# Kernel optimization log

Measured on AMD Instinct MI355X. Metric: run time of the kernel, lower is better.

The kernel has to match this reference:

```python
import jax, jax.numpy as jnp
import numpy as np

# Production-scale 3D conv: B=4, C=64->64, 32^3 volume, 3x3x3 kernel, stride 1, pad 1.
B, CIN, COUT = 4, 64, 64
KSIZE = (3, 3, 3)
STRIDE = (1, 1, 1)
PAD = 1
SPATIAL = (32, 32, 32)


def setup_inputs() -> dict:
    key = jax.random.key(0)
    k1, k2, k3 = jax.random.split(key, 3)
    x = jax.random.normal(k1, (B, CIN) + SPATIAL, dtype=jnp.float32)
    weight = jax.random.normal(k2, (COUT, CIN) + KSIZE, dtype=jnp.float32)
    bias = jax.random.normal(k3, (COUT,), dtype=jnp.float32)
    return {"x": x, "weight": weight, "bias": bias}


def reference(x, weight, bias):
    # The original materializes all sliding-window patches via nested unfold and
    # contracts with einsum('bci...,oci->bo...'). That is exactly a standard
    # cross-correlation (torch-style conv). We express the same math as a direct
    # convolution, avoiding the O(kernel_volume) patch blowup.
    out = jax.lax.conv_general_dilated(
        x,
        weight,
        window_strides=STRIDE,
        padding=[(PAD, PAD)] * 3,
        dimension_numbers=("NCDHW", "OIDHW", "NCDHW"),
    )
    return out + bias.reshape(1, -1, 1, 1, 1)
```

## Files before the change

kernel.cpp:

```cpp
#include <hip/hip_runtime.h>
#include <hip/hip_bf16.h>

#define WS_W_OFF    0
#define WS_ZERO_OFF 221184
#define WS_XT_OFF   262144

typedef __attribute__((ext_vector_type(8)))  short s16x8;
typedef __attribute__((ext_vector_type(4)))  float f32x4;
typedef __attribute__((ext_vector_type(16))) float f32x16;

#define GLOBAL_AS __attribute__((address_space(1)))
#define LDS_AS    __attribute__((address_space(3)))

__device__ __forceinline__ unsigned short f2bf(float f) {
  unsigned u = __builtin_bit_cast(unsigned, f);
  u = u + 0x7fffu + ((u >> 16) & 1u);
  return (unsigned short)(u >> 16);
}

__global__ void prep_kernel(const float* __restrict__ x,
                            const float* __restrict__ w,
                            unsigned short* __restrict__ wsw,
                            float* __restrict__ zeros,
                            unsigned short* __restrict__ xt) {
  int blk = blockIdx.x;
  if (blk < 432) {
    int t = blk * 256 + threadIdx.x;
    int tap  = t % 27;
    int cin  = (t / 27) & 63;
    int cout = t / (27 * 64);
    int h  = cin >> 5;
    int c5 = cin & 31;
    int ks = c5 >> 4;
    int hi = (c5 >> 3) & 1;
    int j  = c5 & 7;
    int nt = cout >> 5;
    int l  = hi * 32 + (cout & 31);
    int f  = nt * 2 + ks;
    int dst = (((tap * 2 + h) * 4 + f) * 64 + l) * 8 + j;
    wsw[dst] = f2bf(w[t]);
    if (t < 64) zeros[t] = 0.0f;
  } else {
    int t  = (blk - 432) * 256 + threadIdx.x;
    int s  = t & 32767;
    int c8 = (t >> 15) & 7;
    int b  = t >> 18;
    const float* src = x + (size_t)(b * 64 + c8 * 8) * 32768 + s;
    s16x8 v;
    #pragma unroll
    for (int k = 0; k < 8; ++k) v[k] = (short)f2bf(src[(size_t)k * 32768]);
    *(s16x8*)(xt + (size_t)(b * 32768 + s) * 64 + c8 * 8) = v;
  }
}

__global__ __launch_bounds__(256, 2) void conv_kernel(const float* __restrict__ bias,
                                                      float* __restrict__ out,
                                                      const char* __restrict__ ws) {
  __shared__ __align__(16) unsigned char halo[52 * 1024];

  const int tid  = threadIdx.x;
  const int lane = tid & 63;
  const int w    = tid >> 6;
  const int logical = (blockIdx.x & 7) * 64 + (blockIdx.x >> 3);
  const int yt = logical & 7, zt = (logical >> 3) & 15, b = logical >> 7;
  const int z0 = zt * 2, y0 = yt * 4;
  const int zo  = w >> 1;
  const int yo2 = (w & 1) * 2;

  const int q31 = lane & 31;
  const int hi  = lane >> 5;

  const int sl_sub   = lane >> 2;
  const int sl_chunk = (lane & 3) ^ ((lane >> 3) & 3);

  auto stage_halo = [&](int h) {
    for (int g = w; g < 52; g += 4) {
      int pos = g * 16 + sl_sub;
      int hz = pos / 204; int rem = pos - hz * 204;
      int hy = rem / 34;  int hx = rem - hy * 34;
      int gz = z0 + hz - 1, gy = y0 + hy - 1, gx = hx - 1;
      bool inb = (pos < 816) & ((unsigned)gz < 32u) &
                 ((unsigned)gy < 32u) & ((unsigned)gx < 32u);
      int s = (gz * 32 + gy) * 32 + gx;
      int src = inb ? (WS_XT_OFF + (b * 32768 + s) * 128 + h * 64 + sl_chunk * 16)
                    : WS_ZERO_OFF;
      __builtin_amdgcn_global_load_lds(
          (const GLOBAL_AS void*)(ws + src),
          (LDS_AS void*)(&halo[g * 1024 + lane * 16]),
          16, 0, 0);
    }
  };

  const s16x8* __restrict__ wfr = (const s16x8*)(ws + WS_W_OFF);

  f32x16 acc[2][2];
  #pragma unroll
  for (int mt = 0; mt < 2; ++mt)
    #pragma unroll
    for (int nt = 0; nt < 2; ++nt)
      #pragma unroll
      for (int r = 0; r < 16; ++r) acc[mt][nt][r] = 0.0f;

  s16x8 Ab[3][4], Bb[3][4];
  const int pA0 = (zo * 6 + yo2) * 34 + q31;
  const int pA1 = pA0 + 34;

  auto loadB = [&](int slot, int h, int tap) {
    #pragma unroll
    for (int f = 0; f < 4; ++f)
      Bb[slot][f] = wfr[((tap * 2 + h) * 4 + f) * 64 + lane];
  };

  auto loadA = [&](int slot, int tap) {
    const int kd = tap / 9, r9 = tap - kd * 9;
    const int kh = r9 / 3, kw = r9 - kh * 3;
    const int d  = (kd * 6 + kh) * 34 + kw;
    #pragma unroll
    for (int mt = 0; mt < 2; ++mt) {
      int p = (mt ? pA1 : pA0) + d;
      #pragma unroll
      for (int ks = 0; ks < 2; ++ks) {
        int swz = ((ks << 1) | hi) ^ ((p >> 1) & 3);
        Ab[slot][mt * 2 + ks] = *(const s16x8*)&halo[(p << 6) + (swz << 4)];
      }
    }
  };

  auto compute = [&](int slot) {
    #pragma unroll
    for (int ks = 0; ks < 2; ++ks)
      #pragma unroll
      for (int mt = 0; mt < 2; ++mt)
        #pragma unroll
        for (int nt = 0; nt < 2; ++nt)
          acc[mt][nt] = __builtin_amdgcn_mfma_f32_32x32x16_bf16(
              Ab[slot][mt * 2 + ks], Bb[slot][nt * 2 + ks], acc[mt][nt], 0, 0, 0);
  };

  auto run27 = [&](int h) {
    loadA(0, 0); loadA(1, 1);
    #pragma unroll
    for (int tap = 0; tap < 27; ++tap) {
      if (tap < 25) {
        loadB((tap + 2) % 3, h, tap + 2);
        loadA((tap + 2) % 3, tap + 2);
      }
      compute(tap % 3);
    }
  };

  stage_halo(0);
  loadB(0, 0, 0); loadB(1, 0, 1);
  __syncthreads();
  run27(0);

  loadB(0, 1, 0); loadB(1, 1, 1);
  __syncthreads();
  stage_halo(1);
  __syncthreads();
  run27(1);

  const int z = z0 + zo;
  #pragma unroll
  for (int nt = 0; nt < 2; ++nt) {
    int cout = nt * 32 + q31;
    float bv = bias[cout];
    #pragma unroll
    for (int mt = 0; mt < 2; ++mt) {
      int y = y0 + yo2 + mt;
      float* orow = out + ((size_t)((b * 64 + cout) * 32 + z) * 32 + y) * 32;
      #pragma unroll
      for (int q = 0; q < 4; ++q) {
        int x0 = q * 8 + hi * 4;
        f32x4 v;
        #pragma unroll
        for (int r = 0; r < 4; ++r) v[r] = acc[mt][nt][q * 4 + r] + bv;
        *(f32x4*)&orow[x0] = v;
      }
    }
  }
}

extern "C" void kernel_launch(void* const* d_in, const int* in_sizes, int n_in,
                              void* d_out, int out_size, void* d_ws, size_t ws_size,
                              hipStream_t stream) {
  const float* x    = (const float*)d_in[0];
  const float* wgt  = (const float*)d_in[1];
  const float* bias = (const float*)d_in[2];
  float* out = (float*)d_out;
  char* ws = (char*)d_ws;

  prep_kernel<<<4528, 256, 0, stream>>>(x, wgt,
                                        (unsigned short*)(ws + WS_W_OFF),
                                        (float*)(ws + WS_ZERO_OFF),
                                        (unsigned short*)(ws + WS_XT_OFF));
  conv_kernel<<<512, 256, 0, stream>>>(bias, out, ws);
}
```

Before: 50.05 us.

## Enlarge conv block tile to 4 z-planes with 8 waves splitting cout halves

Each block now covers 4 z × 4 y rows with 512 threads and 256 blocks. Each wave handles one z row, four y rows and one 32-wide cout half. The larger tile cuts the halo overlap, so less input is re-staged per output. The explicit triple-buffered register prefetch is removed in favour of per-tap loads, with s_setprio raised around the MFMA bursts. In exchange the kernel needs more LDS per block (about 78KB), and with only 256 blocks the grid may under-fill the GPU.

```diff
diff --git a/kernel.cpp b/kernel.cpp
--- a/kernel.cpp
+++ b/kernel.cpp
@@ -53,130 +53,105 @@
   }
 }
 
-__global__ __launch_bounds__(256, 2) void conv_kernel(const float* __restrict__ bias,
+__global__ __launch_bounds__(512, 2) void conv_kernel(const float* __restrict__ bias,
                                                       float* __restrict__ out,
                                                       const char* __restrict__ ws) {
-  __shared__ __align__(16) unsigned char halo[52 * 1024];
+  __shared__ __align__(16) unsigned char halo[1224 * 64];
 
   const int tid  = threadIdx.x;
   const int lane = tid & 63;
   const int w    = tid >> 6;
-  const int logical = (blockIdx.x & 7) * 64 + (blockIdx.x >> 3);
-  const int yt = logical & 7, zt = (logical >> 3) & 15, b = logical >> 7;
-  const int z0 = zt * 2, y0 = yt * 4;
-  const int zo  = w >> 1;
-  const int yo2 = (w & 1) * 2;
+  const int zo   = w >> 1;
+  const int nh   = w & 1;
+  const int logical = (blockIdx.x & 7) * 32 + (blockIdx.x >> 3);
+  const int yq = logical & 7, zq = (logical >> 3) & 7, b = logical >> 6;
+  const int z0 = zq * 4, y0 = yq * 4;
 
   const int q31 = lane & 31;
   const int hi  = lane >> 5;
 
-  const int sl_sub   = lane >> 2;
-  const int sl_chunk = (lane & 3) ^ ((lane >> 3) & 3);
+  const int csrc = ((tid & 3) ^ ((tid >> 3) & 3)) * 16;
 
-  auto stage_halo = [&](int h) {
-    for (int g = w; g < 52; g += 4) {
-      int pos = g * 16 + sl_sub;
-      int hz = pos / 204; int rem = pos - hz * 204;
-      int hy = rem / 34;  int hx = rem - hy * 34;
-      int gz = z0 + hz - 1, gy = y0 + hy - 1, gx = hx - 1;
-      bool inb = (pos < 816) & ((unsigned)gz < 32u) &
-                 ((unsigned)gy < 32u) & ((unsigned)gx < 32u);
-      int s = (gz * 32 + gy) * 32 + gx;
-      int src = inb ? (WS_XT_OFF + (b * 32768 + s) * 128 + h * 64 + sl_chunk * 16)
-                    : WS_ZERO_OFF;
-      __builtin_amdgcn_global_load_lds(
-          (const GLOBAL_AS void*)(ws + src),
-          (LDS_AS void*)(&halo[g * 1024 + lane * 16]),
-          16, 0, 0);
+  auto stage = [&](int h) {
+    #pragma unroll 1
+    for (int r = 0; r < 10; ++r) {
+      int pos = r * 128 + (tid >> 2);
+      if (pos < 1224) {
+        int hz = pos / 204; int rem = pos - hz * 204;
+        int hy = rem / 34;  int hx = rem - hy * 34;
+        int gz = z0 + hz - 1, gy = y0 + hy - 1, gx = hx - 1;
+        bool inb = ((unsigned)gz < 32u) & ((unsigned)gy < 32u) &
+                   ((unsigned)gx < 32u);
+        int s = (gz * 32 + gy) * 32 + gx;
+        int src = inb ? (WS_XT_OFF + (b * 32768 + s) * 128 + h * 64 + csrc)
+                      : WS_ZERO_OFF;
+        __builtin_amdgcn_global_load_lds(
+            (const GLOBAL_AS void*)(ws + src),
+            (LDS_AS void*)(&halo[r * 8192 + tid * 16]),
+            16, 0, 0);
+      }
     }
   };
 
   const s16x8* __restrict__ wfr = (const s16x8*)(ws + WS_W_OFF);
 
-  f32x16 acc[2][2];
+  f32x16 acc[4];
   #pragma unroll
-  for (int mt = 0; mt < 2; ++mt)
+  for (int mt = 0; mt < 4; ++mt)
     #pragma unroll
-    for (int nt = 0; nt < 2; ++nt)
+    for (int r = 0; r < 16; ++r) acc[mt][r] = 0.0f;
+
+  auto run27 = [&](int h) {
+    #pragma unroll
+    for (int tap = 0; tap < 27; ++tap) {
+      const int kd = tap / 9, r9 = tap % 9;
+      const int kh = r9 / 3, kw = r9 % 3;
+      s16x8 Bf[2], Af[4][2];
       #pragma unroll
-      for (int r = 0; r < 16; ++r) acc[mt][nt][r] = 0.0f;
-
-  s16x8 Ab[3][4], Bb[3][4];
-  const int pA0 = (zo * 6 + yo2) * 34 + q31;
-  const int pA1 = pA0 + 34;
-
-  auto loadB = [&](int slot, int h, int tap) {
-    #pragma unroll
-    for (int f = 0; f < 4; ++f)
-      Bb[slot][f] = wfr[((tap * 2 + h) * 4 + f) * 64 + lane];
-  };
-
-  auto loadA = [&](int slot, int tap) {
-    const int kd = tap / 9, r9 = tap - kd * 9;
-    const int kh = r9 / 3, kw = r9 - kh * 3;
-    const int d  = (kd * 6 + kh) * 34 + kw;
-    #pragma unroll
-    for (int mt = 0; mt < 2; ++mt) {
-      int p = (mt ? pA1 : pA0) + d;
+      for (int ks = 0; ks < 2; ++ks)
+        Bf[ks] = wfr[((tap * 2 + h) * 4 + nh * 2 + ks) * 64 + lane];
       #pragma unroll
-      for (int ks = 0; ks < 2; ++ks) {
-        int swz = ((ks << 1) | hi) ^ ((p >> 1) & 3);
-        Ab[slot][mt * 2 + ks] = *(const s16x8*)&halo[(p << 6) + (swz << 4)];
+      for (int mt = 0; mt < 4; ++mt) {
+        int p = ((zo + kd) * 6 + mt + kh) * 34 + kw + q31;
+        #pragma unroll
+        for (int ks = 0; ks < 2; ++ks) {
+          int slot = ((ks << 1) | hi) ^ ((p >> 1) & 3);
+          Af[mt][ks] = *(const s16x8*)&halo[(p << 6) + (slot << 4)];
+        }
       }
+      __builtin_amdgcn_s_setprio(1);
+      #pragma unroll
+      for (int mt = 0; mt < 4; ++mt)
+        #pragma unroll
+        for (int ks = 0; ks < 2; ++ks)
+          acc[mt] = __builtin_amdgcn_mfma_f32_32x32x16_bf16(
+              Af[mt][ks], Bf[ks], acc[mt], 0, 0, 0);
+      __builtin_amdgcn_s_setprio(0);
     }
   };
 
-  auto compute = [&](int slot) {
-    #pragma unroll
-    for (int ks = 0; ks < 2; ++ks)
-      #pragma unroll
-      for (int mt = 0; mt < 2; ++mt)
-        #pragma unroll
-        for (int nt = 0; nt < 2; ++nt)
-          acc[mt][nt] = __builtin_amdgcn_mfma_f32_32x32x16_bf16(
-              Ab[slot][mt * 2 + ks], Bb[slot][nt * 2 + ks], acc[mt][nt], 0, 0, 0);
-  };
-
-  auto run27 = [&](int h) {
-    loadA(0, 0); loadA(1, 1);
-    #pragma unroll
-    for (int tap = 0; tap < 27; ++tap) {
-      if (tap < 25) {
-        loadB((tap + 2) % 3, h, tap + 2);
-        loadA((tap + 2) % 3, tap + 2);
-      }
-      compute(tap % 3);
-    }
-  };
-
-  stage_halo(0);
-  loadB(0, 0, 0); loadB(1, 0, 1);
+  stage(0);
   __syncthreads();
   run27(0);
-
-  loadB(0, 1, 0); loadB(1, 1, 1);
   __syncthreads();
-  stage_halo(1);
+  stage(1);
   __syncthreads();
   run27(1);
 
   const int z = z0 + zo;
+  const int cout = nh * 32 + q31;
+  const float bv = bias[cout];
   #pragma unroll
-  for (int nt = 0; nt < 2; ++nt) {
-    int cout = nt * 32 + q31;
-    float bv = bias[cout];
+  for (int mt = 0; mt < 4; ++mt) {
+    int y = y0 + mt;
+    float* orow = out + ((size_t)((b * 64 + cout) * 32 + z) * 32 + y) * 32;
     #pragma unroll
-    for (int mt = 0; mt < 2; ++mt) {
-      int y = y0 + yo2 + mt;
-      float* orow = out + ((size_t)((b * 64 + cout) * 32 + z) * 32 + y) * 32;
+    for (int q = 0; q < 4; ++q) {
+      int x0 = q * 8 + hi * 4;
+      f32x4 v;
       #pragma unroll
-      for (int q = 0; q < 4; ++q) {
-        int x0 = q * 8 + hi * 4;
-        f32x4 v;
-        #pragma unroll
-        for (int r = 0; r < 4; ++r) v[r] = acc[mt][nt][q * 4 + r] + bv;
-        *(f32x4*)&orow[x0] = v;
-      }
+      for (int r = 0; r < 4; ++r) v[r] = acc[mt][q * 4 + r] + bv;
+      *(f32x4*)&orow[x0] = v;
     }
   }
 }
@@ -194,5 +169,5 @@
                                         (unsigned short*)(ws + WS_W_OFF),
                                         (float*)(ws + WS_ZERO_OFF),
                                         (unsigned short*)(ws + WS_XT_OFF));
-  conv_kernel<<<512, 256, 0, stream>>>(bias, out, ws);
+  conv_kernel<<<256, 512, 0, stream>>>(bias, out, ws);
 }
```

After: 60.29 us. 20.5% more time.
